# Kernel tuning notes

Hardware: AMD Instinct MI355X
Metric: run time of the kernel (lower is better)

## Reference

```python
import jax, jax.numpy as jnp
import numpy as np

N_EMB = 512
DIM = 64
BETA = 0.25
EPS = 1e-10


def setup_inputs() -> dict:
    key = jax.random.key(0)
    k1, k2 = jax.random.split(key)
    z = jax.random.normal(k1, (32, 64, 64, 64), dtype=jnp.float32)  # (B, C=DIM, H, W)
    # embedding weight initialized uniform(-1/K, 1/K) as in the module
    weight = jax.random.uniform(k2, (N_EMB, DIM), dtype=jnp.float32,
                                minval=-1.0 / N_EMB, maxval=1.0 / N_EMB)
    return {"z": z, "weight": weight}


def reference(z, weight):
    # (B,C,H,W) -> (B,H,W,C)
    zp = jnp.transpose(z, (0, 2, 3, 1))
    zf = zp.reshape(-1, DIM)  # (N, D)
    # pairwise squared distances ||z||^2 + ||e||^2 - 2 z.e  -> (N, K)
    d = (jnp.sum(zf * zf, axis=1, keepdims=True)
         + jnp.sum(weight * weight, axis=1)
         - 2.0 * zf @ weight.T)
    codebook = jnp.argmin(d, axis=1)  # (N,)
    encodings = jax.nn.one_hot(codebook, N_EMB, dtype=zf.dtype)  # (N, K)
    # direct gather == one_hot @ weight (same math, efficient form)
    z_q = weight[codebook].reshape(zp.shape)
    sg = jax.lax.stop_gradient
    loss = jnp.mean((sg(z_q) - zp) ** 2) + BETA * jnp.mean((z_q - sg(zp)) ** 2)
    # straight-through estimator
    z_q = zp + sg(z_q - zp)
    e_mean = jnp.mean(encodings, axis=0)
    perplexity = jnp.exp(-jnp.sum(e_mean * jnp.log(e_mean + EPS)))
    z_q = jnp.transpose(z_q, (0, 3, 1, 2))  # back to (B,C,H,W)
    return (loss, z_q, perplexity, encodings, codebook)
```

## Files before the change

kernel.cpp:

```cpp
#include <hip/hip_runtime.h>
#include <math.h>

#define NK 512
#define NPTS (32*64*64)
#define NELEM (32*64*64*64)

#define OFF_LOSS 0
#define OFF_ZQ   1
#define OFF_PERP (1 + NELEM)
#define OFF_ENC  (2 + NELEM)
#define OFF_CB   (2 + NELEM + (size_t)NPTS * NK)

typedef float v2f __attribute__((ext_vector_type(2)));


__global__ __launch_bounds__(256) void vq_prep(const float* __restrict__ wg,
                                               float* __restrict__ wT,
                                               float* __restrict__ bnd) {
    __shared__ float tl[64 * 65];
    const int t = threadIdx.x;
    const int kbase = blockIdx.x * 64;
    #pragma unroll
    for (int it = 0; it < 16; ++it) {
        int i = it * 256 + t;
        int k = i >> 6, d = i & 63;
        tl[k * 65 + d] = wg[(size_t)(kbase + k) * 64 + d];
    }
    __syncthreads();
    #pragma unroll
    for (int it = 0; it < 16; ++it) {
        int j = it * 256 + t;
        int d = j >> 6, kk = j & 63;
        wT[(size_t)d * 512 + kbase + kk] = tl[kk * 65 + d];
    }
    if (t < 64) {
        float s = 0.f;
        #pragma unroll 4
        for (int d = 0; d < 64; ++d) {
            float v = tl[t * 65 + d];
            s = __fadd_rn(s, __fmul_rn(v, v));
        }
        bnd[kbase + t] = s;
    }
}

__global__ __launch_bounds__(256, 2) void vq_main(const float* __restrict__ zg,
                                                  const float* __restrict__ wg,
                                                  const float* __restrict__ wT,
                                                  const float* __restrict__ bndg,
                                                  float* __restrict__ out,
                                                  int* __restrict__ hist,
                                                  double* __restrict__ lossAcc) {
    const int t = threadIdx.x;
    const int blk = blockIdx.x;
    const int b = blk >> 6;
    const int h = blk & 63;

    __shared__ __align__(16) float zt[64 * 64];
    __shared__ __align__(16) float buf[4096];
    __shared__ __align__(16) float r2v[256];
    __shared__ int   r2i[256];
    __shared__ float aRow[64];
    __shared__ int   idxs[64];
    __shared__ float wsum[4];

    float* redv = buf;
    int*   redi = (int*)(buf + 2048);
    float* zqt  = buf;

    {
        const size_t base = (size_t)b * 262144 + (size_t)h * 64;
        const int w2 = (t & 31) * 2;
        const int c0 = t >> 5;
        #pragma unroll
        for (int c = c0; c < 64; c += 8) {
            float2 v = *(const float2*)(zg + base + (size_t)c * 4096 + w2);
            *(float2*)(zt + c * 64 + w2) = v;
        }
    }
    __syncthreads();

    if (t < 64) {
        float s = 0.f;
        for (int d = 0; d < 64; ++d) {
            float v = zt[d * 64 + t];
            s = __fadd_rn(s, __fmul_rn(v, v));
        }
        aRow[t] = s;
    }
    __syncthreads();

    const int tx = t & 7;
    const int ty = t >> 3;
    const int p0 = tx * 8;
    const int k0 = ty * 8;

    float best[8];
    int bidx[8];
    #pragma unroll
    for (int i = 0; i < 8; ++i) { best[i] = INFINITY; bidx[i] = 0; }

    const float* ztp = zt + p0;

    #pragma unroll
    for (int c = 0; c < 2; ++c) {
        v2f acc[8][4];
        #pragma unroll
        for (int i = 0; i < 8; ++i)
            #pragma unroll
            for (int jj = 0; jj < 4; ++jj) acc[i][jj] = (v2f){0.f, 0.f};

        const float* wrow = wT + c * 256 + k0;

        #pragma unroll 4
        for (int d = 0; d < 64; ++d) {
            float4 z0 = *(const float4*)(ztp + d * 64);
            float4 z1 = *(const float4*)(ztp + d * 64 + 4);
            float4 w0 = *(const float4*)(wrow + d * 512);
            float4 w1 = *(const float4*)(wrow + d * 512 + 4);
            const float zr[8] = {z0.x, z0.y, z0.z, z0.w, z1.x, z1.y, z1.z, z1.w};
            v2f wv[4];
            wv[0] = (v2f){w0.x, w0.y}; wv[1] = (v2f){w0.z, w0.w};
            wv[2] = (v2f){w1.x, w1.y}; wv[3] = (v2f){w1.z, w1.w};
            #pragma unroll
            for (int i = 0; i < 8; ++i) {
                v2f zz = (v2f){zr[i], zr[i]};
                #pragma unroll
                for (int jj = 0; jj < 4; ++jj)
                    acc[i][jj] = __builtin_elementwise_fma(zz, wv[jj], acc[i][jj]);
            }
        }

        float bn[8];
        {
            const float4* bp = (const float4*)(bndg + c * 256 + k0);
            float4 b0 = bp[0], b1 = bp[1];
            bn[0] = b0.x; bn[1] = b0.y; bn[2] = b0.z; bn[3] = b0.w;
            bn[4] = b1.x; bn[5] = b1.y; bn[6] = b1.z; bn[7] = b1.w;
        }
        float av[8];
        {
            float4 a0 = *(const float4*)(aRow + p0);
            float4 a1 = *(const float4*)(aRow + p0 + 4);
            av[0] = a0.x; av[1] = a0.y; av[2] = a0.z; av[3] = a0.w;
            av[4] = a1.x; av[5] = a1.y; av[6] = a1.z; av[7] = a1.w;
        }

        #pragma unroll
        for (int i = 0; i < 8; ++i) {
            #pragma unroll
            for (int j = 0; j < 8; ++j) {
                float dotv = acc[i][j >> 1][j & 1];
                float dist = __fsub_rn(__fadd_rn(av[i], bn[j]), 2.0f * dotv);
                int k = c * 256 + k0 + j;
                if (dist < best[i]) { best[i] = dist; bidx[i] = k; }
            }
        }
    }

    #pragma unroll
    for (int i = 0; i < 8; ++i) {
        redv[ty * 64 + p0 + i] = best[i];
        redi[ty * 64 + p0 + i] = bidx[i];
    }
    __syncthreads();

    {
        const int p = t & 63, g = t >> 6;
        float bv = INFINITY; int bi = 0;
        #pragma unroll
        for (int x = g * 8; x < g * 8 + 8; ++x) {
            float v = redv[x * 64 + p];
            int ii = redi[x * 64 + p];
            if (v < bv || (v == bv && ii < bi)) { bv = v; bi = ii; }
        }
        r2v[g * 64 + p] = bv;
        r2i[g * 64 + p] = bi;
    }
    __syncthreads();

    if (t < 64) {
        float bv = r2v[t];
        int bi = r2i[t];
        #pragma unroll
        for (int g = 1; g < 4; ++g) {
            float v = r2v[g * 64 + t];
            int ii = r2i[g * 64 + t];
            if (v < bv || (v == bv && ii < bi)) { bv = v; bi = ii; }
        }
        idxs[t] = bi;
        atomicAdd(&hist[bi], 1);
        out[OFF_CB + (size_t)blk * 64 + t] = (float)bi;
    }
    __syncthreads();

    if (t < 128) {
        const int p = t >> 1, half = t & 1;
        const int bi = idxs[p];
        const float4* wr4 = (const float4*)(wg + (size_t)bi * 64) + half * 8;
        #pragma unroll
        for (int q = 0; q < 8; ++q) {
            float4 v = wr4[q];
            int d = half * 32 + q * 4;
            zqt[(d + 0) * 64 + p] = v.x;
            zqt[(d + 1) * 64 + p] = v.y;
            zqt[(d + 2) * 64 + p] = v.z;
            zqt[(d + 3) * 64 + p] = v.w;
        }
    }

    {
        float4* enc = (float4*)(out + OFF_ENC + (size_t)blk * 64 * NK);
        #pragma unroll
        for (int it = 0; it < 32; ++it) {
            int e = it * 256 + t;
            int r = e >> 7, cc = e & 127;
            int idx = idxs[r];
            float4 v = make_float4(0.f, 0.f, 0.f, 0.f);
            if ((idx >> 2) == cc) ((float*)&v)[idx & 3] = 1.0f;
            enc[(size_t)r * 128 + cc] = v;
        }
    }
    __syncthreads();

    float lsum = 0.f;
    {
        float* zq = out + OFF_ZQ + (size_t)b * 262144 + (size_t)h * 64;
        #pragma unroll
        for (int it = 0; it < 4; ++it) {
            int f = it * 256 + t;
            int d = f >> 4, pp = (f & 15) * 4;
            float4 zv = *(const float4*)(zt + d * 64 + pp);
            float4 qv = *(const float4*)(zqt + d * 64 + pp);
            float4 o;
            float dx = __fsub_rn(qv.x, zv.x); lsum = __fadd_rn(lsum, __fmul_rn(dx, dx)); o.x = __fadd_rn(zv.x, dx);
            float dy = __fsub_rn(qv.y, zv.y); lsum = __fadd_rn(lsum, __fmul_rn(dy, dy)); o.y = __fadd_rn(zv.y, dy);
            float dz = __fsub_rn(qv.z, zv.z); lsum = __fadd_rn(lsum, __fmul_rn(dz, dz)); o.z = __fadd_rn(zv.z, dz);
            float dw = __fsub_rn(qv.w, zv.w); lsum = __fadd_rn(lsum, __fmul_rn(dw, dw)); o.w = __fadd_rn(zv.w, dw);
            *(float4*)(zq + (size_t)d * 4096 + pp) = o;
        }
    }
    #pragma unroll
    for (int off = 32; off > 0; off >>= 1)
        lsum += __shfl_down(lsum, off);
    if ((t & 63) == 0) wsum[t >> 6] = lsum;
    __syncthreads();
    if (t == 0) {
        float tot = (wsum[0] + wsum[1]) + (wsum[2] + wsum[3]);
        atomicAdd(lossAcc, (double)tot);
    }
}

__global__ __launch_bounds__(512) void vq_finalize(const int* __restrict__ hist,
                                                   const double* __restrict__ lossAcc,
                                                   float* __restrict__ out) {
    __shared__ float sh[512];
    const int t = threadIdx.x;
    float p = (float)hist[t] / (float)NPTS;
    sh[t] = __fmul_rn(p, logf(__fadd_rn(p, 1e-10f)));
    __syncthreads();
    for (int s = 256; s > 0; s >>= 1) {
        if (t < s) sh[t] += sh[t + s];
        __syncthreads();
    }
    if (t == 0) {
        float m = (float)(*lossAcc / (double)NELEM);
        out[OFF_LOSS] = __fadd_rn(m, __fmul_rn(0.25f, m));
        out[OFF_PERP] = expf(-sh[0]);
    }
}

extern "C" void kernel_launch(void* const* d_in, const int* in_sizes, int n_in,
                              void* d_out, int out_size, void* d_ws, size_t ws_size,
                              hipStream_t stream) {
    const float* z = (const float*)d_in[0];
    const float* w = (const float*)d_in[1];
    float* out = (float*)d_out;
    int* hist = (int*)d_ws;
    double* lossAcc = (double*)((char*)d_ws + 2048);
    float* wT = (float*)((char*)d_ws + 4096);
    float* bnd = wT + 64 * 512;

    (void)hipMemsetAsync(d_ws, 0, 4096, stream);
    vq_prep<<<8, 256, 0, stream>>>(w, wT, bnd);
    vq_main<<<2048, 256, 0, stream>>>(z, w, wT, bnd, out, hist, lossAcc);
    vq_finalize<<<1, 512, 0, stream>>>(hist, lossAcc, out);
}
```

Before: 438.7 us.

## Split VQ main kernel into assignment and emission kernels to cut LDS

The fused kernel is split into two. vq_assign computes distances and the argmin and writes codebook indices; vq_emit reads those indices back, gathers codebook rows, writes the one-hot encodings and z_q, and accumulates the loss. vq_assign reuses the z tile as its reduction scratch, which removes a 16KB shared buffer and may allow more resident blocks, while the heavy encoding writes move into a separate kernel. The cost is re-reading z (32MB) and the indices from global memory, plus one extra kernel launch.

```diff
diff --git a/kernel.cpp b/kernel.cpp
--- a/kernel.cpp
+++ b/kernel.cpp
@@ -44,29 +44,23 @@
     }
 }
 
-__global__ __launch_bounds__(256, 2) void vq_main(const float* __restrict__ zg,
-                                                  const float* __restrict__ wg,
-                                                  const float* __restrict__ wT,
-                                                  const float* __restrict__ bndg,
-                                                  float* __restrict__ out,
-                                                  int* __restrict__ hist,
-                                                  double* __restrict__ lossAcc) {
+__global__ __launch_bounds__(256, 2) void vq_assign(const float* __restrict__ zg,
+                                                    const float* __restrict__ wT,
+                                                    const float* __restrict__ bndg,
+                                                    float* __restrict__ out,
+                                                    int* __restrict__ hist) {
     const int t = threadIdx.x;
     const int blk = blockIdx.x;
     const int b = blk >> 6;
     const int h = blk & 63;
 
     __shared__ __align__(16) float zt[64 * 64];
-    __shared__ __align__(16) float buf[4096];
     __shared__ __align__(16) float r2v[256];
     __shared__ int   r2i[256];
     __shared__ float aRow[64];
-    __shared__ int   idxs[64];
-    __shared__ float wsum[4];
-
-    float* redv = buf;
-    int*   redi = (int*)(buf + 2048);
-    float* zqt  = buf;
+
+    float* redv = zt;
+    int*   redi = (int*)(zt + 2048);
 
     {
         const size_t base = (size_t)b * 262144 + (size_t)h * 64;
@@ -157,6 +151,7 @@
             }
         }
     }
+    __syncthreads();
 
     #pragma unroll
     for (int i = 0; i < 8; ++i) {
@@ -188,10 +183,26 @@
             int ii = r2i[g * 64 + t];
             if (v < bv || (v == bv && ii < bi)) { bv = v; bi = ii; }
         }
-        idxs[t] = bi;
         atomicAdd(&hist[bi], 1);
         out[OFF_CB + (size_t)blk * 64 + t] = (float)bi;
     }
+}
+
+__global__ __launch_bounds__(256) void vq_emit(const float* __restrict__ zg,
+                                               const float* __restrict__ wg,
+                                               float* __restrict__ out,
+                                               double* __restrict__ lossAcc) {
+    const int t = threadIdx.x;
+    const int blk = blockIdx.x;
+    const int b = blk >> 6;
+    const int h = blk & 63;
+
+    __shared__ __align__(16) float zqt[64 * 64];
+    __shared__ int   idxs[64];
+    __shared__ float wsum[4];
+
+    if (t < 64)
+        idxs[t] = (int)out[OFF_CB + (size_t)blk * 64 + t];
     __syncthreads();
 
     if (t < 128) {
@@ -225,12 +236,14 @@
 
     float lsum = 0.f;
     {
-        float* zq = out + OFF_ZQ + (size_t)b * 262144 + (size_t)h * 64;
+        const size_t base = (size_t)b * 262144 + (size_t)h * 64;
+        const float* zrow = zg + base;
+        float* zq = out + OFF_ZQ + base;
         #pragma unroll
         for (int it = 0; it < 4; ++it) {
             int f = it * 256 + t;
             int d = f >> 4, pp = (f & 15) * 4;
-            float4 zv = *(const float4*)(zt + d * 64 + pp);
+            float4 zv = *(const float4*)(zrow + (size_t)d * 4096 + pp);
             float4 qv = *(const float4*)(zqt + d * 64 + pp);
             float4 o;
             float dx = __fsub_rn(qv.x, zv.x); lsum = __fadd_rn(lsum, __fmul_rn(dx, dx)); o.x = __fadd_rn(zv.x, dx);
@@ -283,6 +296,7 @@
 
     (void)hipMemsetAsync(d_ws, 0, 4096, stream);
     vq_prep<<<8, 256, 0, stream>>>(w, wT, bnd);
-    vq_main<<<2048, 256, 0, stream>>>(z, w, wT, bnd, out, hist, lossAcc);
+    vq_assign<<<2048, 256, 0, stream>>>(z, wT, bnd, out, hist);
+    vq_emit<<<2048, 256, 0, stream>>>(z, w, out, lossAcc);
     vq_finalize<<<1, 512, 0, stream>>>(hist, lossAcc, out);
 }
```

Result: slower. 488.9 us (+11.5%).
